# Optimization experiments

Hardware: AMD Instinct MI355X
Metric: run time of the kernel (lower is better)

Reference implementation:

```python
import jax, jax.numpy as jnp
import numpy as np

N_NODES = 50000
N_EDGES = 800000
IN_DIM = 128
HID = 2 * IN_DIM          # GCNConv out channels = input_dims * 2
FC1 = 1024
FC2 = 512
N_ACT = 16
N_AGENTS = 8192
EPS = 1e-5


def setup_inputs() -> dict:
    key = jax.random.key(0)
    ks = jax.random.split(key, 12)
    def gl(k, shape):  # glorot-ish init for weights
        fan = shape[0]
        return jax.random.normal(k, shape, jnp.float32) / jnp.sqrt(jnp.float32(fan))
    return {
        "x": jax.random.normal(ks[0], (N_NODES, IN_DIM), jnp.float32),
        "edge_index": jax.random.randint(ks[1], (2, N_EDGES), 0, N_NODES, jnp.int32),
        "agent_idx": jax.random.randint(ks[2], (N_AGENTS,), 0, N_NODES, jnp.int32),
        "W_gcn": gl(ks[3], (IN_DIM, HID)),
        "b_gcn": jnp.zeros((HID,), jnp.float32),
        "W1": gl(ks[4], (HID, FC1)),
        "b1": jnp.zeros((FC1,), jnp.float32),
        "g1": jnp.ones((FC1,), jnp.float32),
        "be1": jnp.zeros((FC1,), jnp.float32),
        "W2": gl(ks[5], (FC1, FC2)),
        "b2": jnp.zeros((FC2,), jnp.float32),
        "g2": jnp.ones((FC2,), jnp.float32),
        "be2": jnp.zeros((FC2,), jnp.float32),
        "Wmu": gl(ks[6], (FC2, N_ACT)) * 0.003,
        "bmu": jnp.zeros((N_ACT,), jnp.float32),
    }


def _layernorm(h, g, b):
    mu = jnp.mean(h, axis=-1, keepdims=True)
    var = jnp.mean(jnp.square(h - mu), axis=-1, keepdims=True)
    return (h - mu) * jax.lax.rsqrt(var + EPS) * g + b


def _gcn_conv(x, edge_index, W, b):
    # PyG GCNConv: add self-loops, symmetric normalization, linear, scatter-add.
    n = x.shape[0]
    loop = jnp.arange(n, dtype=edge_index.dtype)
    src = jnp.concatenate([edge_index[0], loop])   # [E+N]
    dst = jnp.concatenate([edge_index[1], loop])   # [E+N]
    deg = jax.ops.segment_sum(jnp.ones_like(dst, jnp.float32), dst, num_segments=n)
    dis = jnp.where(deg > 0, jax.lax.rsqrt(jnp.maximum(deg, 1.0)), 0.0)
    norm = dis[src] * dis[dst]                     # [E+N]
    xw = x @ W                                     # [N, HID]
    msg = xw[src] * norm[:, None]                  # gather + scale
    return jax.ops.segment_sum(msg, dst, num_segments=n) + b


def reference(x, edge_index, agent_idx, W_gcn, b_gcn, W1, b1, g1, be1,
              W2, b2, g2, be2, Wmu, bmu):
    h = _gcn_conv(x, edge_index, W_gcn, b_gcn)     # [N, HID]
    h = h[agent_idx]                               # masked selection -> [A, HID]
    h = jax.nn.relu(h)
    h = jax.nn.relu(_layernorm(h @ W1 + b1, g1, be1))
    h = jax.nn.relu(_layernorm(h @ W2 + b2, g2, be2))
    return jax.nn.sigmoid(h @ Wmu + bmu)           # [A, N_ACT]
```

## Files before the change

kernel.cpp:

```cpp
#include <hip/hip_runtime.h>
#include <hip/hip_bf16.h>
#include <math.h>

#define N_NODES  50000
#define N_EDGES  800000
#define IN_DIM   128
#define HID      256
#define FC1      1024
#define FC2      512
#define N_ACT    16
#define N_AGENTS 8192

#define BK       64
#define LDK      72
#define BM       128
#define BN       128

#define EDGE_BLOCKS ((N_EDGES + 255) / 256)
#define WTR_BLOCKS   208
#define EB_STRIDE    64

typedef short bf16x8 __attribute__((ext_vector_type(8)));
typedef float floatx4 __attribute__((ext_vector_type(4)));

__device__ __forceinline__ unsigned short f2b(float f) {
    union { float f; unsigned int i; } v;
    v.f = f;
    unsigned int lsb = (v.i >> 16) & 1u;
    v.i += 0x7fffu + lsb;
    return (unsigned short)(v.i >> 16);
}

__device__ __forceinline__ float b2f(unsigned short u) {
    union { unsigned int i; float f; } v;
    v.i = ((unsigned int)u) << 16;
    return v.f;
}

__device__ __forceinline__ void wtr_block(int b, int tid,
    const float* __restrict__ Wgcn, const float* __restrict__ W1,
    const float* __restrict__ W2, const float* __restrict__ Wmu,
    unsigned short* __restrict__ wgcn_t, unsigned short* __restrict__ w1_t,
    unsigned short* __restrict__ w2_t, unsigned short* __restrict__ wmu_t,
    unsigned short (*Ts)[72]) {
    const float* src; unsigned short* dstw; int K, N, tk, tn;
    if (b < 8)        { src = Wgcn; dstw = wgcn_t; K = IN_DIM; N = HID;  tk = b >> 2;        tn = b & 3; }
    else if (b < 72)  { int bb = b - 8;  src = W1; dstw = w1_t; K = HID;  N = FC1;  tk = bb >> 4; tn = bb & 15; }
    else if (b < 200) { int bb = b - 72; src = W2; dstw = w2_t; K = FC1;  N = FC2;  tk = bb >> 3; tn = bb & 7; }
    else              { int bb = b - 200; src = Wmu; dstw = wmu_t; K = FC2; N = N_ACT; tk = bb;   tn = 0; }
    int k0 = tk * 64, n0 = tn * 64;
    int r = tid >> 2;
    int cc = (tid & 3) * 16;
    if (n0 + cc < N) {
        const float* p = src + (size_t)(k0 + r) * N + n0 + cc;
        #pragma unroll
        for (int i = 0; i < 16; i += 4) {
            float4 v = *(const float4*)(p + i);
            Ts[r][cc + i + 0] = f2b(v.x);
            Ts[r][cc + i + 1] = f2b(v.y);
            Ts[r][cc + i + 2] = f2b(v.z);
            Ts[r][cc + i + 3] = f2b(v.w);
        }
    }
    __syncthreads();
    int n = tid >> 2;
    if (n0 + n < N) {
        bf16x8 o0, o1;
        #pragma unroll
        for (int i = 0; i < 8; ++i) o0[i] = (short)Ts[cc + i][n];
        #pragma unroll
        for (int i = 0; i < 8; ++i) o1[i] = (short)Ts[cc + 8 + i][n];
        unsigned short* q = dstw + (size_t)(n0 + n) * K + k0 + cc;
        *(bf16x8*)q = o0;
        *(bf16x8*)(q + 8) = o1;
    }
}

__global__ __launch_bounds__(256) void claim_k(const int* __restrict__ agent_idx,
                                               int* __restrict__ nid) {
    int i = blockIdx.x * 256 + threadIdx.x;
    if (i < N_AGENTS) atomicCAS(&nid[agent_idx[i]], 0, i + 1);
}

__global__ __launch_bounds__(256) void edge_k(const int* __restrict__ src,
                                              const int* __restrict__ dst,
                                              const int* __restrict__ nid,
                                              int* __restrict__ deg,
                                              int* __restrict__ fill,
                                              int* __restrict__ ebuf,
                                              const float* __restrict__ Wgcn,
                                              const float* __restrict__ W1,
                                              const float* __restrict__ W2,
                                              const float* __restrict__ Wmu,
                                              unsigned short* __restrict__ wgcn_t,
                                              unsigned short* __restrict__ w1_t,
                                              unsigned short* __restrict__ w2_t,
                                              unsigned short* __restrict__ wmu_t) {
    __shared__ unsigned short Ts[64][72];
    if (blockIdx.x < EDGE_BLOCKS) {
        int e = blockIdx.x * 256 + threadIdx.x;
        if (e >= N_EDGES) return;
        int d = dst[e];
        atomicAdd(&deg[d], 1);
        int cc = nid[d];
        if (cc != 0) {
            int c = cc - 1;
            int p = atomicAdd(&fill[c], 1);
            if (p < EB_STRIDE) ebuf[(c << 6) + p] = src[e];
        }
        return;
    }
    wtr_block(blockIdx.x - EDGE_BLOCKS, threadIdx.x, Wgcn, W1, W2, Wmu,
              wgcn_t, w1_t, w2_t, wmu_t, Ts);
}

__global__ __launch_bounds__(256) void accumx_k(const int* __restrict__ agent_idx,
                                                const int* __restrict__ nid,
                                                const int* __restrict__ fill,
                                                const int* __restrict__ deg,
                                                const int* __restrict__ ebuf,
                                                const float* __restrict__ x,
                                                unsigned short* __restrict__ agg) {
    int c = blockIdx.x * 4 + (threadIdx.x >> 6);
    int lane = threadIdx.x & 63;
    int n = agent_idx[c];
    float ax = 0.0f, ay = 0.0f;
    if (nid[n] == c + 1) {
        int cnt = fill[c];
        if (cnt > EB_STRIDE) cnt = EB_STRIDE;
        float dn = rsqrtf((float)(deg[n] + 1));
        const int* eb = ebuf + (c << 6);
        for (int i = 0; i < cnt; ++i) {
            int s = eb[i];
            float w = rsqrtf((float)(deg[s] + 1)) * dn;
            float2 u = *(const float2*)(x + (size_t)s * IN_DIM + lane * 2);
            ax += w * u.x;
            ay += w * u.y;
        }
        float2 u = *(const float2*)(x + (size_t)n * IN_DIM + lane * 2);
        float w2 = dn * dn;
        ax += w2 * u.x;
        ay += w2 * u.y;
    }
    unsigned int pk = (unsigned int)f2b(ax) | ((unsigned int)f2b(ay) << 16);
    *(unsigned int*)(agg + (size_t)c * IN_DIM + lane * 2) = pk;
}

__global__ __launch_bounds__(256) void gemm_gcn_k(const unsigned short* __restrict__ A,
                                                  const unsigned short* __restrict__ Bt,
                                                  const float* __restrict__ bias,
                                                  unsigned short* __restrict__ outb) {
    __shared__ unsigned short As[64][LDK];
    __shared__ unsigned short Bs[128][LDK];
    int bid = blockIdx.x;
    int tn = (bid >> 3) & 1;
    int tm = (bid & 7) + 8 * (bid >> 4);
    int tid = threadIdx.x;
    int lane = tid & 63, wave = tid >> 6;
    int r16 = lane & 15, quad = lane >> 4;
    int srow = tid >> 2, scol = (tid & 3) * 8;
    const int K = IN_DIM, N = HID;
    const unsigned short* pa0 = A + (size_t)(tm * 64 + srow) * K + scol;
    const unsigned short* pb0 = Bt + (size_t)(tn * 128 + srow) * K + scol;
    const unsigned short* pb1 = Bt + (size_t)(tn * 128 + srow + 64) * K + scol;

    floatx4 acc[4][2];
    #pragma unroll
    for (int i = 0; i < 4; ++i)
        #pragma unroll
        for (int j = 0; j < 2; ++j)
            acc[i][j] = (floatx4){0.0f, 0.0f, 0.0f, 0.0f};

    bf16x8 ra0[2], rb0[2], rb1[2];
    ra0[0] = *(const bf16x8*)pa0;        ra0[1] = *(const bf16x8*)(pa0 + 32);
    rb0[0] = *(const bf16x8*)pb0;        rb0[1] = *(const bf16x8*)(pb0 + 32);
    rb1[0] = *(const bf16x8*)pb1;        rb1[1] = *(const bf16x8*)(pb1 + 32);

    for (int k0 = 0; k0 < K; k0 += BK) {
        *(bf16x8*)&As[srow][scol]           = ra0[0];
        *(bf16x8*)&As[srow][scol + 32]      = ra0[1];
        *(bf16x8*)&Bs[srow][scol]           = rb0[0];
        *(bf16x8*)&Bs[srow][scol + 32]      = rb0[1];
        *(bf16x8*)&Bs[srow + 64][scol]      = rb1[0];
        *(bf16x8*)&Bs[srow + 64][scol + 32] = rb1[1];
        __syncthreads();
        if (k0 + BK < K) {
            ra0[0] = *(const bf16x8*)(pa0 + k0 + BK); ra0[1] = *(const bf16x8*)(pa0 + k0 + BK + 32);
            rb0[0] = *(const bf16x8*)(pb0 + k0 + BK); rb0[1] = *(const bf16x8*)(pb0 + k0 + BK + 32);
            rb1[0] = *(const bf16x8*)(pb1 + k0 + BK); rb1[1] = *(const bf16x8*)(pb1 + k0 + BK + 32);
        }
        #pragma unroll
        for (int h = 0; h < 2; ++h) {
            bf16x8 af[4], bfr[2];
            #pragma unroll
            for (int i = 0; i < 4; ++i)
                af[i] = *(const bf16x8*)&As[i * 16 + r16][h * 32 + quad * 8];
            #pragma unroll
            for (int j = 0; j < 2; ++j)
                bfr[j] = *(const bf16x8*)&Bs[wave * 32 + j * 16 + r16][h * 32 + quad * 8];
            #pragma unroll
            for (int i = 0; i < 4; ++i)
                #pragma unroll
                for (int j = 0; j < 2; ++j)
                    acc[i][j] = __builtin_amdgcn_mfma_f32_16x16x32_bf16(af[i], bfr[j], acc[i][j], 0, 0, 0);
        }
        __syncthreads();
    }

    #pragma unroll
    for (int j = 0; j < 2; ++j) {
        int ocol = tn * 128 + wave * 32 + j * 16 + r16;
        float bv = bias[ocol];
        #pragma unroll
        for (int i = 0; i < 4; ++i) {
            int orow = tm * 64 + i * 16 + quad * 4;
            #pragma unroll
            for (int r = 0; r < 4; ++r) {
                float v = acc[i][j][r] + bv;
                if (v < 0.0f) v = 0.0f;
                outb[(size_t)(orow + r) * N + ocol] = f2b(v);
            }
        }
    }
}

__global__ __launch_bounds__(256) void gemm_fc1_k(const unsigned short* __restrict__ h_node,
                                                  const int* __restrict__ agent,
                                                  const int* __restrict__ nid,
                                                  const unsigned short* __restrict__ Bt,
                                                  const float* __restrict__ bias,
                                                  unsigned short* __restrict__ outb) {
    __shared__ unsigned short As[BM][LDK];
    __shared__ unsigned short Bs[BN][LDK];
    int bid = blockIdx.x;
    int tn = (bid >> 3) & 7;
    int tm = (bid & 7) + 8 * (bid >> 6);
    int tid = threadIdx.x;
    int lane = tid & 63, wave = tid >> 6;
    int wm = wave >> 1, wn = wave & 1;
    int r16 = lane & 15, quad = lane >> 4;
    int srow = tid >> 2, scol = (tid & 3) * 8;
    const int K = HID, N = FC1;
    int c0 = nid[agent[tm * BM + srow]] - 1;
    int c1 = nid[agent[tm * BM + srow + 64]] - 1;
    const unsigned short* pa0 = h_node + (size_t)c0 * K + scol;
    const unsigned short* pa1 = h_node + (size_t)c1 * K + scol;
    const unsigned short* pb0 = Bt + (size_t)(tn * BN + srow) * K + scol;
    const unsigned short* pb1 = Bt + (size_t)(tn * BN + srow + 64) * K + scol;

    floatx4 acc[4][4];
    #pragma unroll
    for (int i = 0; i < 4; ++i)
        #pragma unroll
        for (int j = 0; j < 4; ++j)
            acc[i][j] = (floatx4){0.0f, 0.0f, 0.0f, 0.0f};

    bf16x8 ra0[2], ra1[2], rb0[2], rb1[2];
    ra0[0] = *(const bf16x8*)pa0;        ra0[1] = *(const bf16x8*)(pa0 + 32);
    ra1[0] = *(const bf16x8*)pa1;        ra1[1] = *(const bf16x8*)(pa1 + 32);
    rb0[0] = *(const bf16x8*)pb0;        rb0[1] = *(const bf16x8*)(pb0 + 32);
    rb1[0] = *(const bf16x8*)pb1;        rb1[1] = *(const bf16x8*)(pb1 + 32);

    for (int k0 = 0; k0 < K; k0 += BK) {
        *(bf16x8*)&As[srow][scol]           = ra0[0];
        *(bf16x8*)&As[srow][scol + 32]      = ra0[1];
        *(bf16x8*)&As[srow + 64][scol]      = ra1[0];
        *(bf16x8*)&As[srow + 64][scol + 32] = ra1[1];
        *(bf16x8*)&Bs[srow][scol]           = rb0[0];
        *(bf16x8*)&Bs[srow][scol + 32]      = rb0[1];
        *(bf16x8*)&Bs[srow + 64][scol]      = rb1[0];
        *(bf16x8*)&Bs[srow + 64][scol + 32] = rb1[1];
        __syncthreads();
        if (k0 + BK < K) {
            ra0[0] = *(const bf16x8*)(pa0 + k0 + BK); ra0[1] = *(const bf16x8*)(pa0 + k0 + BK + 32);
            ra1[0] = *(const bf16x8*)(pa1 + k0 + BK); ra1[1] = *(const bf16x8*)(pa1 + k0 + BK + 32);
            rb0[0] = *(const bf16x8*)(pb0 + k0 + BK); rb0[1] = *(const bf16x8*)(pb0 + k0 + BK + 32);
            rb1[0] = *(const bf16x8*)(pb1 + k0 + BK); rb1[1] = *(const bf16x8*)(pb1 + k0 + BK + 32);
        }
        #pragma unroll
        for (int h = 0; h < 2; ++h) {
            bf16x8 af[4], bfr[4];
            #pragma unroll
            for (int i = 0; i < 4; ++i)
                af[i] = *(const bf16x8*)&As[wm * 64 + i * 16 + r16][h * 32 + quad * 8];
            #pragma unroll
            for (int j = 0; j < 4; ++j)
                bfr[j] = *(const bf16x8*)&Bs[wn * 64 + j * 16 + r16][h * 32 + quad * 8];
            #pragma unroll
            for (int i = 0; i < 4; ++i)
                #pragma unroll
                for (int j = 0; j < 4; ++j)
                    acc[i][j] = __builtin_amdgcn_mfma_f32_16x16x32_bf16(af[i], bfr[j], acc[i][j], 0, 0, 0);
        }
        __syncthreads();
    }

    float bvj[4];
    #pragma unroll
    for (int j = 0; j < 4; ++j) bvj[j] = bias[tn * BN + wn * 64 + j * 16 + r16];

    #pragma unroll
    for (int i = 0; i < 4; ++i) {
        #pragma unroll
        for (int r = 0; r < 4; ++r) {
            int orow = tm * BM + wm * 64 + i * 16 + quad * 4 + r;
            #pragma unroll
            for (int j = 0; j < 4; ++j) {
                int ocol = tn * BN + wn * 64 + j * 16 + r16;
                outb[(size_t)orow * N + ocol] = f2b(acc[i][j][r] + bvj[j]);
            }
        }
    }
}

__global__ __launch_bounds__(256) void ln1_k(const unsigned short* __restrict__ zb,
                                             const float* __restrict__ g1,
                                             const float* __restrict__ be1,
                                             unsigned short* __restrict__ zbn) {
    int row = blockIdx.x * 4 + (threadIdx.x >> 6);
    int lane = threadIdx.x & 63;
    const unsigned short* p = zb + (size_t)row * FC1 + lane * 16;
    bf16x8 a0 = *(const bf16x8*)p;
    bf16x8 a1 = *(const bf16x8*)(p + 8);
    float v[16];
    #pragma unroll
    for (int i = 0; i < 8; ++i) {
        v[i]     = b2f((unsigned short)a0[i]);
        v[8 + i] = b2f((unsigned short)a1[i]);
    }
    float s = 0.0f, s2 = 0.0f;
    #pragma unroll
    for (int i = 0; i < 16; ++i) { s += v[i]; s2 += v[i] * v[i]; }
    #pragma unroll
    for (int m = 1; m < 64; m <<= 1) {
        s  += __shfl_xor(s, m);
        s2 += __shfl_xor(s2, m);
    }
    float mean = s * (1.0f / FC1);
    float var = s2 * (1.0f / FC1) - mean * mean;
    float inv = rsqrtf(var + 1e-5f);
    const float4* g4 = (const float4*)(g1 + lane * 16);
    const float4* b4 = (const float4*)(be1 + lane * 16);
    float gg[16], bb[16];
    #pragma unroll
    for (int q = 0; q < 4; ++q) {
        float4 gv = g4[q], bv = b4[q];
        gg[q * 4 + 0] = gv.x; gg[q * 4 + 1] = gv.y; gg[q * 4 + 2] = gv.z; gg[q * 4 + 3] = gv.w;
        bb[q * 4 + 0] = bv.x; bb[q * 4 + 1] = bv.y; bb[q * 4 + 2] = bv.z; bb[q * 4 + 3] = bv.w;
    }
    bf16x8 o0, o1;
    #pragma unroll
    for (int i = 0; i < 8; ++i) {
        float w = (v[i] - mean) * inv * gg[i] + bb[i];
        if (w < 0.0f) w = 0.0f;
        o0[i] = (short)f2b(w);
    }
    #pragma unroll
    for (int i = 0; i < 8; ++i) {
        float w = (v[8 + i] - mean) * inv * gg[8 + i] + bb[8 + i];
        if (w < 0.0f) w = 0.0f;
        o1[i] = (short)f2b(w);
    }
    unsigned short* q = zbn + (size_t)row * FC1 + lane * 16;
    *(bf16x8*)q = o0;
    *(bf16x8*)(q + 8) = o1;
}

__global__ __launch_bounds__(256) void gemm_fc2_k(const unsigned short* __restrict__ A,
                                                  const unsigned short* __restrict__ Bt,
                                                  const float* __restrict__ bias,
                                                  unsigned short* __restrict__ outb) {
    __shared__ unsigned short As[64][LDK];
    __shared__ unsigned short Bs[128][LDK];
    int bid = blockIdx.x;
    int tn = (bid >> 3) & 3;
    int tm = (bid & 7) + 8 * (bid >> 5);
    int tid = threadIdx.x;
    int lane = tid & 63, wave = tid >> 6;
    int r16 = lane & 15, quad = lane >> 4;
    int srow = tid >> 2, scol = (tid & 3) * 8;
    const int K = FC1, N = FC2;
    const unsigned short* pa0 = A + (size_t)(tm * 64 + srow) * K + scol;
    const unsigned short* pb0 = Bt + (size_t)(tn * 128 + srow) * K + scol;
    const unsigned short* pb1 = Bt + (size_t)(tn * 128 + srow + 64) * K + scol;

    floatx4 acc[4][2];
    #pragma unroll
    for (int i = 0; i < 4; ++i)
        #pragma unroll
        for (int j = 0; j < 2; ++j)
            acc[i][j] = (floatx4){0.0f, 0.0f, 0.0f, 0.0f};

    bf16x8 ra0[2], rb0[2], rb1[2];
    ra0[0] = *(const bf16x8*)pa0;        ra0[1] = *(const bf16x8*)(pa0 + 32);
    rb0[0] = *(const bf16x8*)pb0;        rb0[1] = *(const bf16x8*)(pb0 + 32);
    rb1[0] = *(const bf16x8*)pb1;        rb1[1] = *(const bf16x8*)(pb1 + 32);

    for (int k0 = 0; k0 < K; k0 += BK) {
        *(bf16x8*)&As[srow][scol]           = ra0[0];
        *(bf16x8*)&As[srow][scol + 32]      = ra0[1];
        *(bf16x8*)&Bs[srow][scol]           = rb0[0];
        *(bf16x8*)&Bs[srow][scol + 32]      = rb0[1];
        *(bf16x8*)&Bs[srow + 64][scol]      = rb1[0];
        *(bf16x8*)&Bs[srow + 64][scol + 32] = rb1[1];
        __syncthreads();
        if (k0 + BK < K) {
            ra0[0] = *(const bf16x8*)(pa0 + k0 + BK); ra0[1] = *(const bf16x8*)(pa0 + k0 + BK + 32);
            rb0[0] = *(const bf16x8*)(pb0 + k0 + BK); rb0[1] = *(const bf16x8*)(pb0 + k0 + BK + 32);
            rb1[0] = *(const bf16x8*)(pb1 + k0 + BK); rb1[1] = *(const bf16x8*)(pb1 + k0 + BK + 32);
        }
        #pragma unroll
        for (int h = 0; h < 2; ++h) {
            bf16x8 af[4], bfr[2];
            #pragma unroll
            for (int i = 0; i < 4; ++i)
                af[i] = *(const bf16x8*)&As[i * 16 + r16][h * 32 + quad * 8];
            #pragma unroll
            for (int j = 0; j < 2; ++j)
                bfr[j] = *(const bf16x8*)&Bs[wave * 32 + j * 16 + r16][h * 32 + quad * 8];
            #pragma unroll
            for (int i = 0; i < 4; ++i)
                #pragma unroll
                for (int j = 0; j < 2; ++j)
                    acc[i][j] = __builtin_amdgcn_mfma_f32_16x16x32_bf16(af[i], bfr[j], acc[i][j], 0, 0, 0);
        }
        __syncthreads();
    }

    #pragma unroll
    for (int j = 0; j < 2; ++j) {
        int ocol = tn * 128 + wave * 32 + j * 16 + r16;
        float bv = bias[ocol];
        #pragma unroll
        for (int i = 0; i < 4; ++i) {
            int orow = tm * 64 + i * 16 + quad * 4;
            #pragma unroll
            for (int r = 0; r < 4; ++r)
                outb[(size_t)(orow + r) * N + ocol] = f2b(acc[i][j][r] + bv);
        }
    }
}

__global__ __launch_bounds__(256) void ln2head_k(const unsigned short* __restrict__ z,
                                                 const float* __restrict__ g2,
                                                 const float* __restrict__ be2,
                                                 const unsigned short* __restrict__ wmu_t,
                                                 const float* __restrict__ bmu,
                                                 float* __restrict__ out) {
    __shared__ unsigned short Hs[16][520];
    __shared__ float hred[4][64][4];
    int tid = threadIdx.x;
    int tm = blockIdx.x;
    {
        int row = tid >> 4;
        int sub = tid & 15;
        const unsigned short* src = z + (size_t)(tm * 16 + row) * FC2 + sub * 32;
        bf16x8 a0 = *(const bf16x8*)(src);
        bf16x8 a1 = *(const bf16x8*)(src + 8);
        bf16x8 a2 = *(const bf16x8*)(src + 16);
        bf16x8 a3 = *(const bf16x8*)(src + 24);
        float v[32];
        #pragma unroll
        for (int i = 0; i < 8; ++i) {
            v[i]      = b2f((unsigned short)a0[i]);
            v[8 + i]  = b2f((unsigned short)a1[i]);
            v[16 + i] = b2f((unsigned short)a2[i]);
            v[24 + i] = b2f((unsigned short)a3[i]);
        }
        float s = 0.0f, s2 = 0.0f;
        #pragma unroll
        for (int i = 0; i < 32; ++i) { s += v[i]; s2 += v[i] * v[i]; }
        #pragma unroll
        for (int m = 1; m < 16; m <<= 1) {
            s  += __shfl_xor(s, m);
            s2 += __shfl_xor(s2, m);
        }
        float mean = s * (1.0f / FC2);
        float var = s2 * (1.0f / FC2) - mean * mean;
        float inv = rsqrtf(var + 1e-5f);
        #pragma unroll
        for (int i = 0; i < 32; ++i) {
            int c = sub * 32 + i;
            float w = (v[i] - mean) * inv * g2[c] + be2[c];
            if (w < 0.0f) w = 0.0f;
            Hs[row][c] = f2b(w);
        }
    }
    __syncthreads();
    int lane = tid & 63, wave = tid >> 6;
    int r16 = lane & 15, quad = lane >> 4;
    floatx4 acc = {0.0f, 0.0f, 0.0f, 0.0f};
    #pragma unroll
    for (int st = 0; st < 4; ++st) {
        bf16x8 a = *(const bf16x8*)&Hs[r16][wave * 128 + st * 32 + quad * 8];
        bf16x8 b = *(const bf16x8*)(wmu_t + (size_t)r16 * FC2 + wave * 128 + st * 32 + quad * 8);
        acc = __builtin_amdgcn_mfma_f32_16x16x32_bf16(a, b, acc, 0, 0, 0);
    }
    #pragma unroll
    for (int r = 0; r < 4; ++r) hred[wave][lane][r] = acc[r];
    __syncthreads();
    if (wave == 0) {
        #pragma unroll
        for (int r = 0; r < 4; ++r) {
            float v = hred[0][lane][r] + hred[1][lane][r] + hred[2][lane][r] + hred[3][lane][r];
            v += bmu[r16];
            v = 1.0f / (1.0f + expf(-v));
            out[(size_t)(tm * 16 + quad * 4 + r) * N_ACT + r16] = v;
        }
    }
}

extern "C" void kernel_launch(void* const* d_in, const int* in_sizes, int n_in,
                              void* d_out, int out_size, void* d_ws, size_t ws_size,
                              hipStream_t stream) {
    const float* x    = (const float*)d_in[0];
    const int*   ei   = (const int*)d_in[1];
    const int*   agent= (const int*)d_in[2];
    const float* Wgcn = (const float*)d_in[3];
    const float* bgcn = (const float*)d_in[4];
    const float* W1   = (const float*)d_in[5];
    const float* b1   = (const float*)d_in[6];
    const float* g1   = (const float*)d_in[7];
    const float* be1  = (const float*)d_in[8];
    const float* W2   = (const float*)d_in[9];
    const float* b2   = (const float*)d_in[10];
    const float* g2   = (const float*)d_in[11];
    const float* be2  = (const float*)d_in[12];
    const float* Wmu  = (const float*)d_in[13];
    const float* bmu  = (const float*)d_in[14];
    float* out = (float*)d_out;

    const int* srcp = ei;
    const int* dstp = ei + N_EDGES;

    char* ws = (char*)d_ws;
    size_t off = 0;
    char* zero_base = ws;
    int* deg  = (int*)(ws + off);      off += ((size_t)N_NODES * 4 + 255) & ~(size_t)255;
    int* fill = (int*)(ws + off);      off += ((size_t)N_AGENTS * 4 + 255) & ~(size_t)255;
    int* nid  = (int*)(ws + off);      off += ((size_t)N_NODES * 4 + 255) & ~(size_t)255;
    size_t zero_bytes = off;
    int* ebuf = (int*)(ws + off);      off += ((size_t)N_AGENTS * EB_STRIDE * 4 + 255) & ~(size_t)255;
    unsigned short* wgcn_t = (unsigned short*)(ws + off); off += ((size_t)IN_DIM * HID * 2 + 255) & ~(size_t)255;
    unsigned short* w1_t   = (unsigned short*)(ws + off); off += ((size_t)HID * FC1 * 2 + 255) & ~(size_t)255;
    unsigned short* w2_t   = (unsigned short*)(ws + off); off += ((size_t)FC1 * FC2 * 2 + 255) & ~(size_t)255;
    unsigned short* wmu_t  = (unsigned short*)(ws + off); off += ((size_t)FC2 * N_ACT * 2 + 255) & ~(size_t)255;
    unsigned short* agg    = (unsigned short*)(ws + off); off += ((size_t)N_AGENTS * IN_DIM * 2 + 255) & ~(size_t)255;
    unsigned short* h_node = (unsigned short*)(ws + off); off += ((size_t)N_AGENTS * HID * 2 + 255) & ~(size_t)255;
    unsigned short* zb  = (unsigned short*)(ws + off);    off += ((size_t)N_AGENTS * FC1 * 2 + 255) & ~(size_t)255;
    unsigned short* zbn = (unsigned short*)(ws + off);    off += ((size_t)N_AGENTS * FC1 * 2 + 255) & ~(size_t)255;
    unsigned short* zb2 = (unsigned short*)(ws + off);    off += ((size_t)N_AGENTS * FC2 * 2 + 255) & ~(size_t)255;

    hipMemsetAsync(zero_base, 0, zero_bytes, stream);

    claim_k<<<N_AGENTS / 256, 256, 0, stream>>>(agent, nid);

    edge_k<<<EDGE_BLOCKS + WTR_BLOCKS, 256, 0, stream>>>(srcp, dstp, nid, deg, fill, ebuf,
                                                         Wgcn, W1, W2, Wmu,
                                                         wgcn_t, w1_t, w2_t, wmu_t);

    accumx_k<<<N_AGENTS / 4, 256, 0, stream>>>(agent, nid, fill, deg, ebuf, x, agg);

    gemm_gcn_k<<<(HID / 128) * (N_AGENTS / 64), 256, 0, stream>>>(agg, wgcn_t, bgcn, h_node);

    gemm_fc1_k<<<(FC1 / BN) * (N_AGENTS / BM), 256, 0, stream>>>(h_node, agent, nid, w1_t, b1, zb);

    ln1_k<<<N_AGENTS / 4, 256, 0, stream>>>(zb, g1, be1, zbn);

    gemm_fc2_k<<<(FC2 / 128) * (N_AGENTS / 64), 256, 0, stream>>>(zbn, w2_t, b2, zb2);

    ln2head_k<<<N_AGENTS / 16, 256, 0, stream>>>(zb2, g2, be2, wmu_t, bmu, out);
}
```

Baseline: 212.7 us.

## Bucket edges by destination and count degrees with LDS atomics

Replaces the per-edge global atomics for degree counting and agent edge-list filling with a two-pass scheme. The first pass scatters (src,dst) pairs into 256-node destination buckets, using shared-memory histograms and one global atomic per bucket per block. The second pass builds degrees and agent edge lists per bucket with shared-memory atomics. The claim kernel is folded into the scatter launch. This adds a 64-bit pair buffer round-trip and an extra launch, and it silently truncates any bucket that exceeds its fixed capacity.

```diff
diff --git a/kernel.cpp b/kernel.cpp
--- a/kernel.cpp
+++ b/kernel.cpp
@@ -16,9 +16,14 @@
 #define BM       128
 #define BN       128
 
-#define EDGE_BLOCKS ((N_EDGES + 255) / 256)
+#define EB_STRIDE    64
+
+#define SCAT_CHUNK   2048
+#define SCAT_BLOCKS  ((N_EDGES + SCAT_CHUNK - 1) / SCAT_CHUNK)
+#define N_BUCKETS    196
+#define BUCKET_CAP   4608
 #define WTR_BLOCKS   208
-#define EB_STRIDE    64
+#define CLAIM_BLOCKS (N_AGENTS / 256)
 
 typedef short bf16x8 __attribute__((ext_vector_type(8)));
 typedef float floatx4 __attribute__((ext_vector_type(4)));
@@ -76,18 +81,12 @@
     }
 }
 
-__global__ __launch_bounds__(256) void claim_k(const int* __restrict__ agent_idx,
-                                               int* __restrict__ nid) {
-    int i = blockIdx.x * 256 + threadIdx.x;
-    if (i < N_AGENTS) atomicCAS(&nid[agent_idx[i]], 0, i + 1);
-}
-
-__global__ __launch_bounds__(256) void edge_k(const int* __restrict__ src,
+__global__ __launch_bounds__(256) void scat_k(const int* __restrict__ src,
                                               const int* __restrict__ dst,
-                                              const int* __restrict__ nid,
-                                              int* __restrict__ deg,
-                                              int* __restrict__ fill,
-                                              int* __restrict__ ebuf,
+                                              const int* __restrict__ agent_idx,
+                                              int* __restrict__ nid,
+                                              int* __restrict__ bcnt,
+                                              unsigned long long* __restrict__ pairbuf,
                                               const float* __restrict__ Wgcn,
                                               const float* __restrict__ W1,
                                               const float* __restrict__ W2,
@@ -97,26 +96,80 @@
                                               unsigned short* __restrict__ w2_t,
                                               unsigned short* __restrict__ wmu_t) {
     __shared__ unsigned short Ts[64][72];
-    if (blockIdx.x < EDGE_BLOCKS) {
-        int e = blockIdx.x * 256 + threadIdx.x;
-        if (e >= N_EDGES) return;
-        int d = dst[e];
-        atomicAdd(&deg[d], 1);
-        int cc = nid[d];
+    __shared__ int hist[N_BUCKETS], base[N_BUCKETS], cur[N_BUCKETS];
+    int tid = threadIdx.x;
+    int blk = blockIdx.x;
+    if (blk >= SCAT_BLOCKS) {
+        int bb = blk - SCAT_BLOCKS;
+        if (bb < WTR_BLOCKS) {
+            wtr_block(bb, tid, Wgcn, W1, W2, Wmu, wgcn_t, w1_t, w2_t, wmu_t, Ts);
+        } else {
+            int i = (bb - WTR_BLOCKS) * 256 + tid;
+            atomicCAS(&nid[agent_idx[i]], 0, i + 1);
+        }
+        return;
+    }
+    if (tid < N_BUCKETS) { hist[tid] = 0; cur[tid] = 0; }
+    __syncthreads();
+    int e0 = blk * SCAT_CHUNK;
+    int dv[8];
+    #pragma unroll
+    for (int i = 0; i < 8; ++i) {
+        int e = e0 + i * 256 + tid;
+        dv[i] = (e < N_EDGES) ? dst[e] : -1;
+        if (dv[i] >= 0) atomicAdd(&hist[dv[i] >> 8], 1);
+    }
+    __syncthreads();
+    if (tid < N_BUCKETS && hist[tid] > 0)
+        base[tid] = atomicAdd(&bcnt[tid], hist[tid]);
+    __syncthreads();
+    #pragma unroll
+    for (int i = 0; i < 8; ++i) {
+        int e = e0 + i * 256 + tid;
+        if (e < N_EDGES) {
+            int d = dv[i];
+            int bk = d >> 8;
+            int p = base[bk] + atomicAdd(&cur[bk], 1);
+            if (p < BUCKET_CAP)
+                pairbuf[(size_t)bk * BUCKET_CAP + p] =
+                    ((unsigned long long)(unsigned)src[e] << 32) | (unsigned)d;
+        }
+    }
+}
+
+__global__ __launch_bounds__(256) void bucket_k(const int* __restrict__ bcnt,
+                                                const unsigned long long* __restrict__ pairbuf,
+                                                const int* __restrict__ nid,
+                                                int* __restrict__ deg,
+                                                int* __restrict__ ebuf) {
+    __shared__ int nidl[256], lhist[256], lfill[256];
+    int b = blockIdx.x, tid = threadIdx.x;
+    int node = b * 256 + tid;
+    nidl[tid] = (node < N_NODES) ? nid[node] : 0;
+    lhist[tid] = 0;
+    lfill[tid] = 0;
+    __syncthreads();
+    int n = bcnt[b];
+    if (n > BUCKET_CAP) n = BUCKET_CAP;
+    const unsigned long long* pb = pairbuf + (size_t)b * BUCKET_CAP;
+    for (int i = tid; i < n; i += 256) {
+        unsigned long long pr = pb[i];
+        int d = (int)(unsigned)pr;
+        int s = (int)(pr >> 32);
+        int l = d & 255;
+        atomicAdd(&lhist[l], 1);
+        int cc = nidl[l];
         if (cc != 0) {
-            int c = cc - 1;
-            int p = atomicAdd(&fill[c], 1);
-            if (p < EB_STRIDE) ebuf[(c << 6) + p] = src[e];
-        }
-        return;
-    }
-    wtr_block(blockIdx.x - EDGE_BLOCKS, threadIdx.x, Wgcn, W1, W2, Wmu,
-              wgcn_t, w1_t, w2_t, wmu_t, Ts);
+            int p = atomicAdd(&lfill[l], 1);
+            if (p < EB_STRIDE) ebuf[((cc - 1) << 6) + p] = s;
+        }
+    }
+    __syncthreads();
+    if (node < N_NODES) deg[node] = lhist[tid];
 }
 
 __global__ __launch_bounds__(256) void accumx_k(const int* __restrict__ agent_idx,
                                                 const int* __restrict__ nid,
-                                                const int* __restrict__ fill,
                                                 const int* __restrict__ deg,
                                                 const int* __restrict__ ebuf,
                                                 const float* __restrict__ x,
@@ -126,9 +179,10 @@
     int n = agent_idx[c];
     float ax = 0.0f, ay = 0.0f;
     if (nid[n] == c + 1) {
-        int cnt = fill[c];
+        int dn_i = deg[n];
+        int cnt = dn_i;
         if (cnt > EB_STRIDE) cnt = EB_STRIDE;
-        float dn = rsqrtf((float)(deg[n] + 1));
+        float dn = rsqrtf((float)(dn_i + 1));
         const int* eb = ebuf + (c << 6);
         for (int i = 0; i < cnt; ++i) {
             int s = eb[i];
@@ -536,10 +590,12 @@
     char* ws = (char*)d_ws;
     size_t off = 0;
     char* zero_base = ws;
+    int* nid  = (int*)(ws + off);      off += ((size_t)N_NODES * 4 + 255) & ~(size_t)255;
+    int* bcnt = (int*)(ws + off);      off += ((size_t)N_BUCKETS * 4 + 255) & ~(size_t)255;
+    size_t zero_bytes = off;
     int* deg  = (int*)(ws + off);      off += ((size_t)N_NODES * 4 + 255) & ~(size_t)255;
-    int* fill = (int*)(ws + off);      off += ((size_t)N_AGENTS * 4 + 255) & ~(size_t)255;
-    int* nid  = (int*)(ws + off);      off += ((size_t)N_NODES * 4 + 255) & ~(size_t)255;
-    size_t zero_bytes = off;
+    unsigned long long* pairbuf = (unsigned long long*)(ws + off);
+    off += ((size_t)N_BUCKETS * BUCKET_CAP * 8 + 255) & ~(size_t)255;
     int* ebuf = (int*)(ws + off);      off += ((size_t)N_AGENTS * EB_STRIDE * 4 + 255) & ~(size_t)255;
     unsigned short* wgcn_t = (unsigned short*)(ws + off); off += ((size_t)IN_DIM * HID * 2 + 255) & ~(size_t)255;
     unsigned short* w1_t   = (unsigned short*)(ws + off); off += ((size_t)HID * FC1 * 2 + 255) & ~(size_t)255;
@@ -553,13 +609,13 @@
 
     hipMemsetAsync(zero_base, 0, zero_bytes, stream);
 
-    claim_k<<<N_AGENTS / 256, 256, 0, stream>>>(agent, nid);
-
-    edge_k<<<EDGE_BLOCKS + WTR_BLOCKS, 256, 0, stream>>>(srcp, dstp, nid, deg, fill, ebuf,
-                                                         Wgcn, W1, W2, Wmu,
-                                                         wgcn_t, w1_t, w2_t, wmu_t);
-
-    accumx_k<<<N_AGENTS / 4, 256, 0, stream>>>(agent, nid, fill, deg, ebuf, x, agg);
+    scat_k<<<SCAT_BLOCKS + WTR_BLOCKS + CLAIM_BLOCKS, 256, 0, stream>>>(
+        srcp, dstp, agent, nid, bcnt, pairbuf,
+        Wgcn, W1, W2, Wmu, wgcn_t, w1_t, w2_t, wmu_t);
+
+    bucket_k<<<N_BUCKETS, 256, 0, stream>>>(bcnt, pairbuf, nid, deg, ebuf);
+
+    accumx_k<<<N_AGENTS / 4, 256, 0, stream>>>(agent, nid, deg, ebuf, x, agg);
 
     gemm_gcn_k<<<(HID / 128) * (N_AGENTS / 64), 256, 0, stream>>>(agg, wgcn_t, bgcn, h_node);
 
```

Result: faster. 188.5 us (-11.4%).
